# Kernel tuning notes

Hardware: AMD Instinct MI355X
Metric: run time of the kernel (lower is better)

Reference implementation:

```python
import jax, jax.numpy as jnp
import numpy as np

B = 1024
IN = 512      # in_features
O = 64        # out_features
E = 8         # ensamble
K = O * E     # total tiny MLPs, index k = i*E + j (i: output, j: ensemble)


def setup_inputs() -> dict:
    key = jax.random.key(0)
    k1, k2, k3, k4, k5 = jax.random.split(key, 5)
    s = 1.0 / np.sqrt(IN)
    X = jax.random.normal(k1, (B, IN), dtype=jnp.float32)
    # Stacked weights for all K = O*E tiny MLPs.
    # nn.Linear(in,in): y = x @ W1^T + b1, W1: [in_out, in_in]
    W1 = jax.random.uniform(k2, (K, IN, IN), jnp.float32, -s, s)
    b1 = jax.random.uniform(k3, (K, IN), jnp.float32, -s, s)
    # nn.Linear(in,1): W2 squeezed to [K, IN], b2 to [K]
    W2 = jax.random.uniform(k4, (K, IN), jnp.float32, -s, s)
    b2 = jax.random.uniform(k5, (K,), jnp.float32, -s, s)
    return {"X": X, "W1": W1, "b1": b1, "W2": W2, "b2": b2}


def reference(X, W1, b1, W2, b2):
    # h[b,k,:] = relu(X[b] @ W1[k].T + b1[k])  -- one batched GEMM
    h = jax.nn.relu(jnp.einsum('bi,kji->bkj', X, W1) + b1)  # [B,K,IN]
    out = jnp.einsum('bkj,kj->bk', h, W2) + b2              # [B,K]
    # original: concat over ensemble (dim=-1) then stack over out_features (dim=-1)
    out = out.reshape(X.shape[0], O, E).transpose(0, 2, 1)  # [B,E,O]
    return out
```

## Files before the change

kernel.cpp:

```cpp
#include <hip/hip_runtime.h>
#include <hip/hip_bf16.h>

typedef __attribute__((ext_vector_type(8))) short short8;
typedef __attribute__((ext_vector_type(4))) float f32x4;

__device__ __forceinline__ short8 pack8(const f32x4& a, const f32x4& b) {
    union { __hip_bfloat162 h[4]; short8 s; } u;
    u.h[0] = __float22bfloat162_rn(make_float2(a[0], a[1]));
    u.h[1] = __float22bfloat162_rn(make_float2(a[2], a[3]));
    u.h[2] = __float22bfloat162_rn(make_float2(b[0], b[1]));
    u.h[3] = __float22bfloat162_rn(make_float2(b[2], b[3]));
    return u.s;
}

__device__ __forceinline__ int swz(int g) { return g ^ (((g >> 4) & 3) << 1); }

#define PHASE(P, KTV, SET, DOW, DOI, VM)                                          \
  do {                                                                            \
    const char* rb_ = smem + ((KTV) & 1) * 65536;                                 \
    _Pragma("unroll") for (int ii = 0; ii < 4; ++ii)                              \
        av[ii] = *(const short8*)(rb_ +                                           \
            (((wm * 8 + ((P) & 1) * 4 + ii) * 2 + ((P) >> 1)) << 10) + rdo);      \
    if (((P) & 1) == 0) {                                                         \
      _Pragma("unroll") for (int pp = 0; pp < 4; ++pp)                            \
          bv[pp] = *(const short8*)(rb_ + 32768 +                                 \
              (((wn * 4 + pp) * 2 + ((P) >> 1)) << 10) + rdo);                    \
    }                                                                             \
    if (DOW) {                                                                    \
      asm volatile("s_waitcnt vmcnt(" #VM ")" ::: "memory");                      \
      short8 w0_ = pack8(SET[0], SET[1]);                                         \
      short8 w1_ = pack8(SET[2], SET[3]);                                         \
      char* wdst_ = smem + (((KTV) + 1) & 1) * 65536 +                            \
                    (((P) >= 2) ? 32768 : 0) + (((P) & 1) * 16384) + wfrag;       \
      *(short8*)wdst_ = w0_;                                                      \
      *(short8*)(wdst_ + 1024) = w1_;                                             \
    }                                                                             \
    if (DOI) {                                                                    \
      const float* isrc_ = (((P) >= 2) ? (As + ((KTV) + 2) * 64)                  \
                                       : (Bs + ((KTV) + 1) * 64)) +               \
                           (((P) & 1) ? 65536 : 0);                               \
      SET[0] = *(const f32x4*)isrc_;                                              \
      SET[1] = *(const f32x4*)(isrc_ + 4);                                        \
      SET[2] = *(const f32x4*)(isrc_ + 32);                                       \
      SET[3] = *(const f32x4*)(isrc_ + 36);                                       \
    }                                                                             \
    asm volatile("s_waitcnt lgkmcnt(0)" ::: "memory");                            \
    __builtin_amdgcn_sched_barrier(0);                                            \
    __builtin_amdgcn_s_barrier();                                                 \
    __builtin_amdgcn_s_setprio(1);                                                \
    _Pragma("unroll") for (int ii = 0; ii < 4; ++ii)                              \
        _Pragma("unroll") for (int pp = 0; pp < 4; ++pp)                          \
            acc[((P) & 1) * 4 + ii][pp] = __builtin_amdgcn_mfma_f32_16x16x32_bf16(\
                av[ii], bv[pp], acc[((P) & 1) * 4 + ii][pp], 0, 0, 0);            \
    __builtin_amdgcn_s_setprio(0);                                                \
    __builtin_amdgcn_sched_barrier(0);                                            \
  } while (0)

__global__ __launch_bounds__(512, 2)
void ens_mlp_kernel(const float* __restrict__ X,
                    const float* __restrict__ W1,
                    const float* __restrict__ B1,
                    const float* __restrict__ W2,
                    const float* __restrict__ B2,
                    float* __restrict__ out)
{
    extern __shared__ char smem[];
    const int t    = threadIdx.x;
    const int lane = t & 63;
    const int wv   = t >> 6;
    const int wm   = wv >> 2;
    const int wn   = wv & 3;

    const int bb  = blockIdx.x;
    const int xcd = bb & 7;
    const int j   = bb >> 3;
    const int km  = xcd * 64 + (j >> 3);
    const int sub = j & 7;
    const int mt  = sub >> 1;
    const int nt  = sub & 1;

    const float* __restrict__ W1k = W1 + (size_t)km * (512 * 512);

    const int lr = t >> 2;
    const int c  = t & 3;
    const float* As = X   + (size_t)(mt * 256 + lr) * 512 + c * 8;
    const float* Bs = W1k + (size_t)(nt * 256 + lr) * 512 + c * 8;
    const int wfrag = ((lr >> 4) << 11) + (swz((c << 4) | (lr & 15)) << 4);
    const int rdo   = swz(lane) << 4;

    f32x4 s0[4], s1[4];
    {
        f32x4 t0[4], t1[4], t2[4], t3[4];
        const float* q0 = As;
        const float* q1 = As + 65536;
        const float* q2 = Bs;
        const float* q3 = Bs + 65536;
        t0[0]=*(const f32x4*)q0; t0[1]=*(const f32x4*)(q0+4); t0[2]=*(const f32x4*)(q0+32); t0[3]=*(const f32x4*)(q0+36);
        t1[0]=*(const f32x4*)q1; t1[1]=*(const f32x4*)(q1+4); t1[2]=*(const f32x4*)(q1+32); t1[3]=*(const f32x4*)(q1+36);
        t2[0]=*(const f32x4*)q2; t2[1]=*(const f32x4*)(q2+4); t2[2]=*(const f32x4*)(q2+32); t2[3]=*(const f32x4*)(q2+36);
        t3[0]=*(const f32x4*)q3; t3[1]=*(const f32x4*)(q3+4); t3[2]=*(const f32x4*)(q3+32); t3[3]=*(const f32x4*)(q3+36);
        asm volatile("s_waitcnt vmcnt(12)" ::: "memory");
        { short8 a=pack8(t0[0],t0[1]), b=pack8(t0[2],t0[3]);
          char* d = smem + 0     + wfrag; *(short8*)d=a; *(short8*)(d+1024)=b; }
        asm volatile("s_waitcnt vmcnt(8)" ::: "memory");
        { short8 a=pack8(t1[0],t1[1]), b=pack8(t1[2],t1[3]);
          char* d = smem + 16384 + wfrag; *(short8*)d=a; *(short8*)(d+1024)=b; }
        asm volatile("s_waitcnt vmcnt(4)" ::: "memory");
        { short8 a=pack8(t2[0],t2[1]), b=pack8(t2[2],t2[3]);
          char* d = smem + 32768 + wfrag; *(short8*)d=a; *(short8*)(d+1024)=b; }
        asm volatile("s_waitcnt vmcnt(0)" ::: "memory");
        { short8 a=pack8(t3[0],t3[1]), b=pack8(t3[2],t3[3]);
          char* d = smem + 49152 + wfrag; *(short8*)d=a; *(short8*)(d+1024)=b; }
        const float* q4 = As + 64;
        const float* q5 = As + 64 + 65536;
        s0[0]=*(const f32x4*)q4; s0[1]=*(const f32x4*)(q4+4); s0[2]=*(const f32x4*)(q4+32); s0[3]=*(const f32x4*)(q4+36);
        s1[0]=*(const f32x4*)q5; s1[1]=*(const f32x4*)(q5+4); s1[2]=*(const f32x4*)(q5+32); s1[3]=*(const f32x4*)(q5+36);
        asm volatile("s_waitcnt lgkmcnt(0)" ::: "memory");
        __builtin_amdgcn_sched_barrier(0);
        __builtin_amdgcn_s_barrier();
    }

    f32x4 acc[8][4];
#pragma unroll
    for (int i = 0; i < 8; ++i)
#pragma unroll
        for (int p = 0; p < 4; ++p)
            acc[i][p] = (f32x4)0.0f;

    short8 av[4], bv[4];

#pragma unroll 1
    for (int kt = 0; kt < 6; ++kt) {
        PHASE(0, kt, s0, true, true, 4);
        PHASE(1, kt, s1, true, true, 4);
        PHASE(2, kt, s0, true, true, 4);
        PHASE(3, kt, s1, true, true, 4);
    }
    PHASE(0, 6, s0, true, true, 4);
    PHASE(1, 6, s1, true, true, 4);
    PHASE(2, 6, s0, true, false, 4);
    PHASE(3, 6, s1, true, false, 0);
    PHASE(0, 7, s0, false, false, 0);
    PHASE(1, 7, s1, false, false, 0);
    PHASE(2, 7, s0, false, false, 0);
    PHASE(3, 7, s1, false, false, 0);

    const int nc = lane & 15;
    const int kq = lane >> 4;
    float b1v[4], w2v[4];
#pragma unroll
    for (int pp = 0; pp < 4; ++pp) {
        int n = nt * 256 + wn * 64 + pp * 16 + nc;
        b1v[pp] = B1[km * 512 + n];
        w2v[pp] = W2[km * 512 + n];
    }

    float* lout = (float*)smem;
#pragma unroll
    for (int i = 0; i < 8; ++i) {
#pragma unroll
        for (int r = 0; r < 4; ++r) {
            float s = 0.f;
#pragma unroll
            for (int pp = 0; pp < 4; ++pp) {
                float h = acc[i][pp][r] + b1v[pp];
                h = h > 0.f ? h : 0.f;
                s += h * w2v[pp];
            }
#pragma unroll
            for (int d = 1; d < 16; d <<= 1)
                s += __shfl_xor(s, d, 64);
            if (nc == 0) {
                int row = wm * 128 + i * 16 + kq * 4 + r;
                lout[row * 4 + wn] = s;
            }
        }
    }
    __syncthreads();
    if (t < 256) {
        float s = lout[t * 4 + 0] + lout[t * 4 + 1] + lout[t * 4 + 2] + lout[t * 4 + 3];
        if (nt == 0) s += B2[km];
        int b = mt * 256 + t;
        atomicAdd(out + (size_t)b * 512 + (km & 7) * 64 + (km >> 3), s);
    }
}

extern "C" void kernel_launch(void* const* d_in, const int* in_sizes, int n_in,
                              void* d_out, int out_size, void* d_ws, size_t ws_size,
                              hipStream_t stream) {
    const float* X  = (const float*)d_in[0];
    const float* W1 = (const float*)d_in[1];
    const float* B1 = (const float*)d_in[2];
    const float* W2 = (const float*)d_in[3];
    const float* B2 = (const float*)d_in[4];
    float* out = (float*)d_out;

    hipMemsetAsync(out, 0, (size_t)out_size * sizeof(float), stream);
    ens_mlp_kernel<<<dim3(4096), dim3(512), 131072, stream>>>(X, W1, B1, W2, B2, out);
}
```

Measured before the change: 420.7 us.

## Halve block to 256 threads with 128x128 per-wave tiles

Moves from 8 waves per block, each computing 128x64, to 4 waves per block, each computing 128x128. Every thread now loads and stages twice as many global elements per phase, and B-fragment reuse from LDS goes up. The cost is a doubled accumulator count (128 floats), which raises register pressure and may force a single wave per SIMD. Fewer waves are left to hide latency, and spills become possible.

```diff
diff --git a/kernel.cpp b/kernel.cpp
--- a/kernel.cpp
+++ b/kernel.cpp
@@ -22,18 +22,22 @@
         av[ii] = *(const short8*)(rb_ +                                           \
             (((wm * 8 + ((P) & 1) * 4 + ii) * 2 + ((P) >> 1)) << 10) + rdo);      \
     if (((P) & 1) == 0) {                                                         \
-      _Pragma("unroll") for (int pp = 0; pp < 4; ++pp)                            \
+      _Pragma("unroll") for (int pp = 0; pp < 8; ++pp)                            \
           bv[pp] = *(const short8*)(rb_ + 32768 +                                 \
-              (((wn * 4 + pp) * 2 + ((P) >> 1)) << 10) + rdo);                    \
+              (((wn * 8 + pp) * 2 + ((P) >> 1)) << 10) + rdo);                    \
     }                                                                             \
     if (DOW) {                                                                    \
       asm volatile("s_waitcnt vmcnt(" #VM ")" ::: "memory");                      \
       short8 w0_ = pack8(SET[0], SET[1]);                                         \
       short8 w1_ = pack8(SET[2], SET[3]);                                         \
+      short8 w2_ = pack8(SET[4], SET[5]);                                         \
+      short8 w3_ = pack8(SET[6], SET[7]);                                         \
       char* wdst_ = smem + (((KTV) + 1) & 1) * 65536 +                            \
                     (((P) >= 2) ? 32768 : 0) + (((P) & 1) * 16384) + wfrag;       \
       *(short8*)wdst_ = w0_;                                                      \
       *(short8*)(wdst_ + 1024) = w1_;                                             \
+      *(short8*)(wdst_ + 8192) = w2_;                                             \
+      *(short8*)(wdst_ + 9216) = w3_;                                             \
     }                                                                             \
     if (DOI) {                                                                    \
       const float* isrc_ = (((P) >= 2) ? (As + ((KTV) + 2) * 64)                  \
@@ -43,20 +47,33 @@
       SET[1] = *(const f32x4*)(isrc_ + 4);                                        \
       SET[2] = *(const f32x4*)(isrc_ + 32);                                       \
       SET[3] = *(const f32x4*)(isrc_ + 36);                                       \
+      SET[4] = *(const f32x4*)(isrc_ + 32768);                                    \
+      SET[5] = *(const f32x4*)(isrc_ + 32772);                                    \
+      SET[6] = *(const f32x4*)(isrc_ + 32800);                                    \
+      SET[7] = *(const f32x4*)(isrc_ + 32804);                                    \
     }                                                                             \
     asm volatile("s_waitcnt lgkmcnt(0)" ::: "memory");                            \
     __builtin_amdgcn_sched_barrier(0);                                            \
     __builtin_amdgcn_s_barrier();                                                 \
     __builtin_amdgcn_s_setprio(1);                                                \
     _Pragma("unroll") for (int ii = 0; ii < 4; ++ii)                              \
-        _Pragma("unroll") for (int pp = 0; pp < 4; ++pp)                          \
+        _Pragma("unroll") for (int pp = 0; pp < 8; ++pp)                          \
             acc[((P) & 1) * 4 + ii][pp] = __builtin_amdgcn_mfma_f32_16x16x32_bf16(\
                 av[ii], bv[pp], acc[((P) & 1) * 4 + ii][pp], 0, 0, 0);            \
     __builtin_amdgcn_s_setprio(0);                                                \
     __builtin_amdgcn_sched_barrier(0);                                            \
   } while (0)
 
-__global__ __launch_bounds__(512, 2)
+#define PRO_WRITE(TT, ROFF)                                                       \
+  do {                                                                            \
+    short8 a_ = pack8(TT[0], TT[1]);                                              \
+    short8 b_ = pack8(TT[2], TT[3]);                                              \
+    char* d_ = smem + (ROFF) + wfrag;                                             \
+    *(short8*)d_ = a_;                                                            \
+    *(short8*)(d_ + 1024) = b_;                                                   \
+  } while (0)
+
+__global__ __launch_bounds__(256, 1)
 void ens_mlp_kernel(const float* __restrict__ X,
                     const float* __restrict__ W1,
                     const float* __restrict__ B1,
@@ -68,8 +85,8 @@
     const int t    = threadIdx.x;
     const int lane = t & 63;
     const int wv   = t >> 6;
-    const int wm   = wv >> 2;
-    const int wn   = wv & 3;
+    const int wm   = wv >> 1;
+    const int wn   = wv & 1;
 
     const int bb  = blockIdx.x;
     const int xcd = bb & 7;
@@ -88,57 +105,60 @@
     const int wfrag = ((lr >> 4) << 11) + (swz((c << 4) | (lr & 15)) << 4);
     const int rdo   = swz(lane) << 4;
 
-    f32x4 s0[4], s1[4];
+    f32x4 s0[8], s1[8];
     {
-        f32x4 t0[4], t1[4], t2[4], t3[4];
-        const float* q0 = As;
-        const float* q1 = As + 65536;
-        const float* q2 = Bs;
-        const float* q3 = Bs + 65536;
-        t0[0]=*(const f32x4*)q0; t0[1]=*(const f32x4*)(q0+4); t0[2]=*(const f32x4*)(q0+32); t0[3]=*(const f32x4*)(q0+36);
-        t1[0]=*(const f32x4*)q1; t1[1]=*(const f32x4*)(q1+4); t1[2]=*(const f32x4*)(q1+32); t1[3]=*(const f32x4*)(q1+36);
-        t2[0]=*(const f32x4*)q2; t2[1]=*(const f32x4*)(q2+4); t2[2]=*(const f32x4*)(q2+32); t2[3]=*(const f32x4*)(q2+36);
-        t3[0]=*(const f32x4*)q3; t3[1]=*(const f32x4*)(q3+4); t3[2]=*(const f32x4*)(q3+32); t3[3]=*(const f32x4*)(q3+36);
-        asm volatile("s_waitcnt vmcnt(12)" ::: "memory");
-        { short8 a=pack8(t0[0],t0[1]), b=pack8(t0[2],t0[3]);
-          char* d = smem + 0     + wfrag; *(short8*)d=a; *(short8*)(d+1024)=b; }
-        asm volatile("s_waitcnt vmcnt(8)" ::: "memory");
-        { short8 a=pack8(t1[0],t1[1]), b=pack8(t1[2],t1[3]);
-          char* d = smem + 16384 + wfrag; *(short8*)d=a; *(short8*)(d+1024)=b; }
-        asm volatile("s_waitcnt vmcnt(4)" ::: "memory");
-        { short8 a=pack8(t2[0],t2[1]), b=pack8(t2[2],t2[3]);
-          char* d = smem + 32768 + wfrag; *(short8*)d=a; *(short8*)(d+1024)=b; }
-        asm volatile("s_waitcnt vmcnt(0)" ::: "memory");
-        { short8 a=pack8(t3[0],t3[1]), b=pack8(t3[2],t3[3]);
-          char* d = smem + 49152 + wfrag; *(short8*)d=a; *(short8*)(d+1024)=b; }
-        const float* q4 = As + 64;
-        const float* q5 = As + 64 + 65536;
-        s0[0]=*(const f32x4*)q4; s0[1]=*(const f32x4*)(q4+4); s0[2]=*(const f32x4*)(q4+32); s0[3]=*(const f32x4*)(q4+36);
-        s1[0]=*(const f32x4*)q5; s1[1]=*(const f32x4*)(q5+4); s1[2]=*(const f32x4*)(q5+32); s1[3]=*(const f32x4*)(q5+36);
+        f32x4 t0[4], t1[4], t2[4], t3[4], t4[4], t5[4], t6[4], t7[4];
+        const float* q;
+        q = As;          t0[0]=*(const f32x4*)q; t0[1]=*(const f32x4*)(q+4); t0[2]=*(const f32x4*)(q+32); t0[3]=*(const f32x4*)(q+36);
+        q = As + 32768;  t1[0]=*(const f32x4*)q; t1[1]=*(const f32x4*)(q+4); t1[2]=*(const f32x4*)(q+32); t1[3]=*(const f32x4*)(q+36);
+        q = As + 65536;  t2[0]=*(const f32x4*)q; t2[1]=*(const f32x4*)(q+4); t2[2]=*(const f32x4*)(q+32); t2[3]=*(const f32x4*)(q+36);
+        q = As + 98304;  t3[0]=*(const f32x4*)q; t3[1]=*(const f32x4*)(q+4); t3[2]=*(const f32x4*)(q+32); t3[3]=*(const f32x4*)(q+36);
+        q = Bs;          t4[0]=*(const f32x4*)q; t4[1]=*(const f32x4*)(q+4); t4[2]=*(const f32x4*)(q+32); t4[3]=*(const f32x4*)(q+36);
+        q = Bs + 32768;  t5[0]=*(const f32x4*)q; t5[1]=*(const f32x4*)(q+4); t5[2]=*(const f32x4*)(q+32); t5[3]=*(const f32x4*)(q+36);
+        q = Bs + 65536;  t6[0]=*(const f32x4*)q; t6[1]=*(const f32x4*)(q+4); t6[2]=*(const f32x4*)(q+32); t6[3]=*(const f32x4*)(q+36);
+        q = Bs + 98304;  t7[0]=*(const f32x4*)q; t7[1]=*(const f32x4*)(q+4); t7[2]=*(const f32x4*)(q+32); t7[3]=*(const f32x4*)(q+36);
+        asm volatile("s_waitcnt vmcnt(28)" ::: "memory"); PRO_WRITE(t0, 0);
+        asm volatile("s_waitcnt vmcnt(24)" ::: "memory"); PRO_WRITE(t1, 8192);
+        asm volatile("s_waitcnt vmcnt(20)" ::: "memory"); PRO_WRITE(t2, 16384);
+        asm volatile("s_waitcnt vmcnt(16)" ::: "memory"); PRO_WRITE(t3, 24576);
+        asm volatile("s_waitcnt vmcnt(12)" ::: "memory"); PRO_WRITE(t4, 32768);
+        asm volatile("s_waitcnt vmcnt(8)"  ::: "memory"); PRO_WRITE(t5, 40960);
+        asm volatile("s_waitcnt vmcnt(4)"  ::: "memory"); PRO_WRITE(t6, 49152);
+        asm volatile("s_waitcnt vmcnt(0)"  ::: "memory"); PRO_WRITE(t7, 57344);
+        q = As + 64;
+        s0[0]=*(const f32x4*)q;         s0[1]=*(const f32x4*)(q+4);
+        s0[2]=*(const f32x4*)(q+32);    s0[3]=*(const f32x4*)(q+36);
+        s0[4]=*(const f32x4*)(q+32768); s0[5]=*(const f32x4*)(q+32772);
+        s0[6]=*(const f32x4*)(q+32800); s0[7]=*(const f32x4*)(q+32804);
+        q = As + 64 + 65536;
+        s1[0]=*(const f32x4*)q;         s1[1]=*(const f32x4*)(q+4);
+        s1[2]=*(const f32x4*)(q+32);    s1[3]=*(const f32x4*)(q+36);
+        s1[4]=*(const f32x4*)(q+32768); s1[5]=*(const f32x4*)(q+32772);
+        s1[6]=*(const f32x4*)(q+32800); s1[7]=*(const f32x4*)(q+32804);
         asm volatile("s_waitcnt lgkmcnt(0)" ::: "memory");
         __builtin_amdgcn_sched_barrier(0);
         __builtin_amdgcn_s_barrier();
     }
 
-    f32x4 acc[8][4];
+    f32x4 acc[8][8];
 #pragma unroll
     for (int i = 0; i < 8; ++i)
 #pragma unroll
-        for (int p = 0; p < 4; ++p)
+        for (int p = 0; p < 8; ++p)
             acc[i][p] = (f32x4)0.0f;
 
-    short8 av[4], bv[4];
+    short8 av[4], bv[8];
 
 #pragma unroll 1
     for (int kt = 0; kt < 6; ++kt) {
-        PHASE(0, kt, s0, true, true, 4);
-        PHASE(1, kt, s1, true, true, 4);
-        PHASE(2, kt, s0, true, true, 4);
-        PHASE(3, kt, s1, true, true, 4);
-    }
-    PHASE(0, 6, s0, true, true, 4);
-    PHASE(1, 6, s1, true, true, 4);
-    PHASE(2, 6, s0, true, false, 4);
+        PHASE(0, kt, s0, true, true, 8);
+        PHASE(1, kt, s1, true, true, 8);
+        PHASE(2, kt, s0, true, true, 8);
+        PHASE(3, kt, s1, true, true, 8);
+    }
+    PHASE(0, 6, s0, true, true, 8);
+    PHASE(1, 6, s1, true, true, 8);
+    PHASE(2, 6, s0, true, false, 8);
     PHASE(3, 6, s1, true, false, 0);
     PHASE(0, 7, s0, false, false, 0);
     PHASE(1, 7, s1, false, false, 0);
@@ -147,10 +167,10 @@
 
     const int nc = lane & 15;
     const int kq = lane >> 4;
-    float b1v[4], w2v[4];
-#pragma unroll
-    for (int pp = 0; pp < 4; ++pp) {
-        int n = nt * 256 + wn * 64 + pp * 16 + nc;
+    float b1v[8], w2v[8];
+#pragma unroll
+    for (int pp = 0; pp < 8; ++pp) {
+        int n = nt * 256 + (wn * 8 + pp) * 16 + nc;
         b1v[pp] = B1[km * 512 + n];
         w2v[pp] = W2[km * 512 + n];
     }
@@ -162,7 +182,7 @@
         for (int r = 0; r < 4; ++r) {
             float s = 0.f;
 #pragma unroll
-            for (int pp = 0; pp < 4; ++pp) {
+            for (int pp = 0; pp < 8; ++pp) {
                 float h = acc[i][pp][r] + b1v[pp];
                 h = h > 0.f ? h : 0.f;
                 s += h * w2v[pp];
@@ -172,13 +192,13 @@
                 s += __shfl_xor(s, d, 64);
             if (nc == 0) {
                 int row = wm * 128 + i * 16 + kq * 4 + r;
-                lout[row * 4 + wn] = s;
+                lout[row * 2 + wn] = s;
             }
         }
     }
     __syncthreads();
-    if (t < 256) {
-        float s = lout[t * 4 + 0] + lout[t * 4 + 1] + lout[t * 4 + 2] + lout[t * 4 + 3];
+    {
+        float s = lout[t * 2 + 0] + lout[t * 2 + 1];
         if (nt == 0) s += B2[km];
         int b = mt * 256 + t;
         atomicAdd(out + (size_t)b * 512 + (km & 7) * 64 + (km >> 3), s);
@@ -196,5 +216,5 @@
     float* out = (float*)d_out;
 
     hipMemsetAsync(out, 0, (size_t)out_size * sizeof(float), stream);
-    ens_mlp_kernel<<<dim3(4096), dim3(512), 131072, stream>>>(X, W1, B1, W2, B2, out);
+    ens_mlp_kernel<<<dim3(4096), dim3(256), 131072, stream>>>(X, W1, B1, W2, B2, out);
 }
```

Measured after the change: 1.598 ms. 280% more time.

## Restructure main loop into two K-substeps with one barrier per tile

Applied to the files above, without the earlier changes.

Replaces the four-phase software pipeline, which had a barrier per phase and staged loads half a tile at a time, with a per-tile loop. Each iteration issues the next tile's W1 global loads, runs a full 8x4 MFMA block on the first K half, writes the converted W1 to the other LDS buffer, then repeats for X with the second K half, ending in a single barrier. The aim is fewer barriers and larger MFMA bursts. In exchange it raises register pressure (8 A fragments plus 8 staged float4 vectors) and waits on vmcnt(0) right after each MFMA burst, which may expose global load latency.

```diff
diff --git a/kernel.cpp b/kernel.cpp
--- a/kernel.cpp
+++ b/kernel.cpp
@@ -13,47 +13,53 @@
     return u.s;
 }
 
-__device__ __forceinline__ int swz(int g) { return g ^ (((g >> 4) & 3) << 1); }
+__device__ __forceinline__ int swz(int g) { return g ^ (((g >> 4) & 3) << 4 >> 3); }
+__device__ __forceinline__ int swz4(int g) { return g ^ (((g >> 4) & 3) << 1); }
 
-#define PHASE(P, KTV, SET, DOW, DOI, VM)                                          \
-  do {                                                                            \
-    const char* rb_ = smem + ((KTV) & 1) * 65536;                                 \
-    _Pragma("unroll") for (int ii = 0; ii < 4; ++ii)                              \
-        av[ii] = *(const short8*)(rb_ +                                           \
-            (((wm * 8 + ((P) & 1) * 4 + ii) * 2 + ((P) >> 1)) << 10) + rdo);      \
-    if (((P) & 1) == 0) {                                                         \
-      _Pragma("unroll") for (int pp = 0; pp < 4; ++pp)                            \
-          bv[pp] = *(const short8*)(rb_ + 32768 +                                 \
-              (((wn * 4 + pp) * 2 + ((P) >> 1)) << 10) + rdo);                    \
-    }                                                                             \
-    if (DOW) {                                                                    \
-      asm volatile("s_waitcnt vmcnt(" #VM ")" ::: "memory");                      \
-      short8 w0_ = pack8(SET[0], SET[1]);                                         \
-      short8 w1_ = pack8(SET[2], SET[3]);                                         \
-      char* wdst_ = smem + (((KTV) + 1) & 1) * 65536 +                            \
-                    (((P) >= 2) ? 32768 : 0) + (((P) & 1) * 16384) + wfrag;       \
-      *(short8*)wdst_ = w0_;                                                      \
-      *(short8*)(wdst_ + 1024) = w1_;                                             \
-    }                                                                             \
-    if (DOI) {                                                                    \
-      const float* isrc_ = (((P) >= 2) ? (As + ((KTV) + 2) * 64)                  \
-                                       : (Bs + ((KTV) + 1) * 64)) +               \
-                           (((P) & 1) ? 65536 : 0);                               \
-      SET[0] = *(const f32x4*)isrc_;                                              \
-      SET[1] = *(const f32x4*)(isrc_ + 4);                                        \
-      SET[2] = *(const f32x4*)(isrc_ + 32);                                       \
-      SET[3] = *(const f32x4*)(isrc_ + 36);                                       \
-    }                                                                             \
-    asm volatile("s_waitcnt lgkmcnt(0)" ::: "memory");                            \
-    __builtin_amdgcn_sched_barrier(0);                                            \
-    __builtin_amdgcn_s_barrier();                                                 \
-    __builtin_amdgcn_s_setprio(1);                                                \
-    _Pragma("unroll") for (int ii = 0; ii < 4; ++ii)                              \
-        _Pragma("unroll") for (int pp = 0; pp < 4; ++pp)                          \
-            acc[((P) & 1) * 4 + ii][pp] = __builtin_amdgcn_mfma_f32_16x16x32_bf16(\
-                av[ii], bv[pp], acc[((P) & 1) * 4 + ii][pp], 0, 0, 0);            \
-    __builtin_amdgcn_s_setprio(0);                                                \
-    __builtin_amdgcn_sched_barrier(0);                                            \
+
+#define ISSUE(S, BASE, KT1)                                                   \
+  do {                                                                        \
+    const float* q_ = (BASE) + (KT1) * 64;                                    \
+    S[0] = *(const f32x4*)q_;          S[1] = *(const f32x4*)(q_ + 4);        \
+    S[2] = *(const f32x4*)(q_ + 32);   S[3] = *(const f32x4*)(q_ + 36);       \
+    const float* q2_ = q_ + 65536;                                            \
+    S[4] = *(const f32x4*)q2_;         S[5] = *(const f32x4*)(q2_ + 4);       \
+    S[6] = *(const f32x4*)(q2_ + 32);  S[7] = *(const f32x4*)(q2_ + 36);      \
+  } while (0)
+
+#define WRITEB(S, WB, OPOFF)                                                  \
+  do {                                                                        \
+    char* d0_ = (WB) + (OPOFF) + wfrag;                                       \
+    *(short8*)d0_ = pack8(S[0], S[1]);                                        \
+    *(short8*)(d0_ + 1024) = pack8(S[2], S[3]);                               \
+    char* d1_ = d0_ + 16384;                                                  \
+    *(short8*)d1_ = pack8(S[4], S[5]);                                        \
+    *(short8*)(d1_ + 1024) = pack8(S[6], S[7]);                               \
+  } while (0)
+
+#define KK(RB, KKV)                                                           \
+  do {                                                                        \
+    _Pragma("unroll") for (int mi = 0; mi < 8; ++mi)                          \
+        av[mi] = *(const short8*)((RB) +                                      \
+            (((wm * 8 + mi) * 2 + (KKV)) << 10) + rdo);                       \
+    _Pragma("unroll") for (int pp = 0; pp < 4; ++pp)                          \
+        bv[pp] = *(const short8*)((RB) + 32768 +                              \
+            (((wn * 4 + pp) * 2 + (KKV)) << 10) + rdo);                       \
+    __builtin_amdgcn_s_setprio(1);                                            \
+    _Pragma("unroll") for (int mi = 0; mi < 8; ++mi)                          \
+        _Pragma("unroll") for (int pp = 0; pp < 4; ++pp)                      \
+            acc[mi][pp] = __builtin_amdgcn_mfma_f32_16x16x32_bf16(            \
+                av[mi], bv[pp], acc[mi][pp], 0, 0, 0);                        \
+    __builtin_amdgcn_s_setprio(0);                                            \
+  } while (0)
+
+#define PRO_WRITE(TT, ROFF)                                                   \
+  do {                                                                        \
+    short8 a_ = pack8(TT[0], TT[1]);                                          \
+    short8 b_ = pack8(TT[2], TT[3]);                                          \
+    char* d_ = smem + (ROFF) + wfrag;                                         \
+    *(short8*)d_ = a_;                                                        \
+    *(short8*)(d_ + 1024) = b_;                                               \
   } while (0)
 
 __global__ __launch_bounds__(512, 2)
@@ -85,36 +91,20 @@
     const int c  = t & 3;
     const float* As = X   + (size_t)(mt * 256 + lr) * 512 + c * 8;
     const float* Bs = W1k + (size_t)(nt * 256 + lr) * 512 + c * 8;
-    const int wfrag = ((lr >> 4) << 11) + (swz((c << 4) | (lr & 15)) << 4);
-    const int rdo   = swz(lane) << 4;
+    const int wfrag = ((lr >> 4) << 11) + (swz4((c << 4) | (lr & 15)) << 4);
+    const int rdo   = swz4(lane) << 4;
 
-    f32x4 s0[4], s1[4];
     {
         f32x4 t0[4], t1[4], t2[4], t3[4];
-        const float* q0 = As;
-        const float* q1 = As + 65536;
-        const float* q2 = Bs;
-        const float* q3 = Bs + 65536;
-        t0[0]=*(const f32x4*)q0; t0[1]=*(const f32x4*)(q0+4); t0[2]=*(const f32x4*)(q0+32); t0[3]=*(const f32x4*)(q0+36);
-        t1[0]=*(const f32x4*)q1; t1[1]=*(const f32x4*)(q1+4); t1[2]=*(const f32x4*)(q1+32); t1[3]=*(const f32x4*)(q1+36);
-        t2[0]=*(const f32x4*)q2; t2[1]=*(const f32x4*)(q2+4); t2[2]=*(const f32x4*)(q2+32); t2[3]=*(const f32x4*)(q2+36);
-        t3[0]=*(const f32x4*)q3; t3[1]=*(const f32x4*)(q3+4); t3[2]=*(const f32x4*)(q3+32); t3[3]=*(const f32x4*)(q3+36);
-        asm volatile("s_waitcnt vmcnt(12)" ::: "memory");
-        { short8 a=pack8(t0[0],t0[1]), b=pack8(t0[2],t0[3]);
-          char* d = smem + 0     + wfrag; *(short8*)d=a; *(short8*)(d+1024)=b; }
-        asm volatile("s_waitcnt vmcnt(8)" ::: "memory");
-        { short8 a=pack8(t1[0],t1[1]), b=pack8(t1[2],t1[3]);
-          char* d = smem + 16384 + wfrag; *(short8*)d=a; *(short8*)(d+1024)=b; }
-        asm volatile("s_waitcnt vmcnt(4)" ::: "memory");
-        { short8 a=pack8(t2[0],t2[1]), b=pack8(t2[2],t2[3]);
-          char* d = smem + 32768 + wfrag; *(short8*)d=a; *(short8*)(d+1024)=b; }
-        asm volatile("s_waitcnt vmcnt(0)" ::: "memory");
-        { short8 a=pack8(t3[0],t3[1]), b=pack8(t3[2],t3[3]);
-          char* d = smem + 49152 + wfrag; *(short8*)d=a; *(short8*)(d+1024)=b; }
-        const float* q4 = As + 64;
-        const float* q5 = As + 64 + 65536;
-        s0[0]=*(const f32x4*)q4; s0[1]=*(const f32x4*)(q4+4); s0[2]=*(const f32x4*)(q4+32); s0[3]=*(const f32x4*)(q4+36);
-        s1[0]=*(const f32x4*)q5; s1[1]=*(const f32x4*)(q5+4); s1[2]=*(const f32x4*)(q5+32); s1[3]=*(const f32x4*)(q5+36);
+        const float* q;
+        q = As;          t0[0]=*(const f32x4*)q; t0[1]=*(const f32x4*)(q+4); t0[2]=*(const f32x4*)(q+32); t0[3]=*(const f32x4*)(q+36);
+        q = As + 65536;  t1[0]=*(const f32x4*)q; t1[1]=*(const f32x4*)(q+4); t1[2]=*(const f32x4*)(q+32); t1[3]=*(const f32x4*)(q+36);
+        q = Bs;          t2[0]=*(const f32x4*)q; t2[1]=*(const f32x4*)(q+4); t2[2]=*(const f32x4*)(q+32); t2[3]=*(const f32x4*)(q+36);
+        q = Bs + 65536;  t3[0]=*(const f32x4*)q; t3[1]=*(const f32x4*)(q+4); t3[2]=*(const f32x4*)(q+32); t3[3]=*(const f32x4*)(q+36);
+        asm volatile("s_waitcnt vmcnt(12)" ::: "memory"); PRO_WRITE(t0, 0);
+        asm volatile("s_waitcnt vmcnt(8)"  ::: "memory"); PRO_WRITE(t1, 16384);
+        asm volatile("s_waitcnt vmcnt(4)"  ::: "memory"); PRO_WRITE(t2, 32768);
+        asm volatile("s_waitcnt vmcnt(0)"  ::: "memory"); PRO_WRITE(t3, 49152);
         asm volatile("s_waitcnt lgkmcnt(0)" ::: "memory");
         __builtin_amdgcn_sched_barrier(0);
         __builtin_amdgcn_s_barrier();
@@ -127,30 +117,38 @@
         for (int p = 0; p < 4; ++p)
             acc[i][p] = (f32x4)0.0f;
 
-    short8 av[4], bv[4];
+    short8 av[8], bv[4];
+    f32x4 sS[8];
 
 #pragma unroll 1
-    for (int kt = 0; kt < 6; ++kt) {
-        PHASE(0, kt, s0, true, true, 4);
-        PHASE(1, kt, s1, true, true, 4);
-        PHASE(2, kt, s0, true, true, 4);
-        PHASE(3, kt, s1, true, true, 4);
+    for (int kt = 0; kt < 7; ++kt) {
+        const char* rb = smem + (kt & 1) * 65536;
+        char* wb       = smem + ((kt + 1) & 1) * 65536;
+
+        ISSUE(sS, Bs, kt + 1);
+        KK(rb, 0);
+        asm volatile("s_waitcnt vmcnt(0)" ::: "memory");
+        WRITEB(sS, wb, 32768);
+        ISSUE(sS, As, kt + 1);
+        KK(rb, 1);
+        asm volatile("s_waitcnt vmcnt(0)" ::: "memory");
+        WRITEB(sS, wb, 0);
+        asm volatile("s_waitcnt lgkmcnt(0)" ::: "memory");
+        __builtin_amdgcn_sched_barrier(0);
+        __builtin_amdgcn_s_barrier();
     }
-    PHASE(0, 6, s0, true, true, 4);
-    PHASE(1, 6, s1, true, true, 4);
-    PHASE(2, 6, s0, true, false, 4);
-    PHASE(3, 6, s1, true, false, 0);
-    PHASE(0, 7, s0, false, false, 0);
-    PHASE(1, 7, s1, false, false, 0);
-    PHASE(2, 7, s0, false, false, 0);
-    PHASE(3, 7, s1, false, false, 0);
+    {
+        const char* rb = smem + 65536;
+        KK(rb, 0);
+        KK(rb, 1);
+    }
 
     const int nc = lane & 15;
     const int kq = lane >> 4;
     float b1v[4], w2v[4];
 #pragma unroll
     for (int pp = 0; pp < 4; ++pp) {
-        int n = nt * 256 + wn * 64 + pp * 16 + nc;
+        int n = nt * 256 + (wn * 4 + pp) * 16 + nc;
         b1v[pp] = B1[km * 512 + n];
         w2v[pp] = W2[km * 512 + n];
     }
```

Result: no change. 428.2 us (+1.8%).
